# Performance work log

Measured on AMD Instinct MI355X. Metric: run time of the kernel, lower is better.

The kernel has to match this reference:

```python
import jax, jax.numpy as jnp
import numpy as np

N = 50000
E = 800000
D = 256
EPS = 1e-5  # BatchNorm eps


def _gcn_conv(x, W, b, row, col):
    # PyG GCNConv: h = x @ W; add self-loops; sym-normalize; scatter-add; + bias
    h = x @ W  # [N, D]
    deg = jnp.zeros((N,), x.dtype).at[col].add(jnp.ones((row.shape[0],), x.dtype))
    dinv = jax.lax.rsqrt(deg)  # deg >= 1 thanks to self-loops
    norm = dinv[row] * dinv[col]  # [E+N]
    msg = h[row] * norm[:, None]  # gather + scale, [E+N, D]
    out = jnp.zeros_like(h).at[col].add(msg)  # scatter-aggregate
    return out + b


def _bn(x, gamma, beta):
    # BatchNorm1d in training mode: batch statistics over nodes
    m = jnp.mean(x, axis=0)
    v = jnp.var(x, axis=0)
    return (x - m) * jax.lax.rsqrt(v + EPS) * gamma + beta


def setup_inputs() -> dict:
    key = jax.random.key(0)
    ks = jax.random.split(key, 4)
    x = jax.random.normal(ks[0], (N, D), dtype=jnp.float32)
    edge_index = jax.random.randint(ks[1], (2, E), 0, N, dtype=jnp.int64)
    s = 1.0 / np.sqrt(D)
    W1 = jax.random.uniform(ks[2], (D, D), jnp.float32, -s, s)
    W2 = jax.random.uniform(ks[3], (D, D), jnp.float32, -s, s)
    z = jnp.zeros((D,), jnp.float32)
    o = jnp.ones((D,), jnp.float32)
    return {"x": x, "edge_index": edge_index,
            "W1": W1, "b1": z, "g1": o, "be1": z,
            "W2": W2, "b2": z, "g2": o, "be2": z}


def reference(x, edge_index, W1, b1, g1, be1, W2, b2, g2, be2):
    loops = jnp.arange(N, dtype=edge_index.dtype)
    row = jnp.concatenate([edge_index[0], loops])  # sources
    col = jnp.concatenate([edge_index[1], loops])  # targets
    # layer 1: GCNConv -> BN -> ReLU (dropout is identity in eval)
    h = _gcn_conv(x, W1, b1, row, col)
    h = jax.nn.relu(_bn(h, g1, be1))
    # layer 2
    h = _gcn_conv(h, W2, b2, row, col)
    h = jax.nn.relu(_bn(h, g2, be2))
    return h
```

## Files before the change

kernel.cpp:

```cpp
#include <hip/hip_runtime.h>
#include <cstdint>
#include <cstddef>

constexpr int N = 50000;
constexpr int E = 800000;
constexpr int D = 256;
constexpr float EPS = 1e-5f;
constexpr int NB = (N + 255) / 256;
constexpr int BN_BLOCKS = 512;
constexpr int GB = (N + 63) / 64;

typedef __attribute__((ext_vector_type(8))) short short8;
typedef __attribute__((ext_vector_type(4))) float f32x4;

__device__ __forceinline__ unsigned short f2bf(float f) {
  union { float f; unsigned u; } c; c.f = f;
  unsigned u = c.u;
  u += 0x7fff + ((u >> 16) & 1);
  return (unsigned short)(u >> 16);
}
__device__ __forceinline__ float bf2f(unsigned short h) {
  union { unsigned u; float f; } c; c.u = ((unsigned)h) << 16;
  return c.f;
}

__global__ void k_detect(const void* __restrict__ ei, int* __restrict__ flag) {
  int t = threadIdx.x;
  const int* p = (const int*)ei;
  int nz = 0;
  for (int i = 2 * t + 1; i < 2048; i += 128) nz |= (p[i] != 0);
  unsigned long long b = __ballot(nz != 0);
  if (t == 0) *flag = (b == 0ULL) ? 1 : 0;
}

__device__ __forceinline__ int edge_at(const void* ei, int is64, long long pos) {
  if (is64) return (int)((const long long*)ei)[pos];
  return ((const int*)ei)[pos];
}

__global__ void k_count(const void* __restrict__ ei, const int* __restrict__ flag,
                        int* __restrict__ degc) {
  int e = blockIdx.x * 256 + threadIdx.x;
  if (e >= E) return;
  int is64 = *flag;
  int c = edge_at(ei, is64, (long long)E + e);
  atomicAdd(&degc[c], 1);
}

__global__ void k_scan_partial(const int* __restrict__ degc, int* __restrict__ bsum,
                               float* __restrict__ dinv) {
  __shared__ int sd[256];
  int t = threadIdx.x;
  int i = blockIdx.x * 256 + t;
  int dv = (i < N) ? degc[i] : 0;
  if (i < N) dinv[i] = rsqrtf((float)(dv + 1));
  int v = (i < N) ? (dv + 1) : 0;
  sd[t] = v;
  __syncthreads();
  for (int s = 128; s > 0; s >>= 1) {
    if (t < s) sd[t] += sd[t + s];
    __syncthreads();
  }
  if (t == 0) bsum[blockIdx.x] = sd[0];
}

__global__ void k_scan_block(int* __restrict__ bsum) {
  __shared__ int sd[256];
  int t = threadIdx.x;
  int v = (t < NB) ? bsum[t] : 0;
  sd[t] = v;
  __syncthreads();
  for (int off = 1; off < 256; off <<= 1) {
    int x = (t >= off) ? sd[t - off] : 0;
    __syncthreads();
    sd[t] += x;
    __syncthreads();
  }
  if (t < NB) bsum[t] = sd[t] - v;
}

__global__ void k_scan_final(const int* __restrict__ degc, const int* __restrict__ bsum,
                             const float* __restrict__ dinv, int* __restrict__ offs,
                             int* __restrict__ curs, int* __restrict__ esrc,
                             float* __restrict__ enrm) {
  __shared__ int sd[256];
  int t = threadIdx.x;
  int i = blockIdx.x * 256 + t;
  int v = (i < N) ? (degc[i] + 1) : 0;
  sd[t] = v;
  __syncthreads();
  for (int off = 1; off < 256; off <<= 1) {
    int x = (t >= off) ? sd[t - off] : 0;
    __syncthreads();
    sd[t] += x;
    __syncthreads();
  }
  if (i < N) {
    int o = bsum[blockIdx.x] + sd[t] - v;
    offs[i] = o;
    curs[i] = o + 1;
    esrc[o] = i;
    float d = dinv[i];
    enrm[o] = d * d;
  }
  if (i == N - 1) offs[N] = bsum[blockIdx.x] + sd[t];
}

__global__ void k_fill_edges(const void* __restrict__ ei, const int* __restrict__ flag,
                             const float* __restrict__ dinv, int* __restrict__ curs,
                             int* __restrict__ esrc, float* __restrict__ enrm) {
  int e = blockIdx.x * 256 + threadIdx.x;
  if (e >= E) return;
  int is64 = *flag;
  int r = edge_at(ei, is64, e);
  int c = edge_at(ei, is64, (long long)E + e);
  int p = atomicAdd(&curs[c], 1);
  esrc[p] = r;
  enrm[p] = dinv[r] * dinv[c];
}

__global__ void k_wfrag(const float* __restrict__ W, unsigned short* __restrict__ Wf) {
  int tile = blockIdx.x;
  int lane = threadIdx.x;
  int kstep = tile >> 4, wn = tile & 15;
  int kbase = kstep * 32 + (lane >> 4) * 8;
  int col = wn * 16 + (lane & 15);
  short8 v;
#pragma unroll
  for (int j = 0; j < 8; ++j)
    v[j] = (short)f2bf(W[(size_t)(kbase + j) * 256 + col]);
  *(short8*)&Wf[(((size_t)tile) * 64 + lane) * 8] = v;
}

template <bool A_BF16, bool FUSE_BN>
__global__ __launch_bounds__(256) void k_gemm(const void* __restrict__ Ap,
                                              const unsigned short* __restrict__ Wf,
                                              unsigned short* __restrict__ C,
                                              const float* __restrict__ sc,
                                              const float* __restrict__ sh) {
  __shared__ unsigned short As[64][40];
  __shared__ unsigned short Cs[64][264];
  int t = threadIdx.x;
  int lane = t & 63;
  int w = t >> 6;
  int row0 = blockIdx.x * 64;
  int l16 = lane & 15, lk = lane >> 4;

  f32x4 acc[4][4];
#pragma unroll
  for (int i = 0; i < 4; ++i)
#pragma unroll
    for (int j = 0; j < 4; ++j) acc[i][j] = (f32x4){0.f, 0.f, 0.f, 0.f};

  int arow = t >> 2;
  int akc = (t & 3) * 8;

  for (int ks = 0; ks < 8; ++ks) {
    {
      int gr = row0 + arow;
      float f[8] = {0.f, 0.f, 0.f, 0.f, 0.f, 0.f, 0.f, 0.f};
      if (gr < N) {
        if (A_BF16) {
          const unsigned short* A = (const unsigned short*)Ap;
          short8 v = *(const short8*)&A[(size_t)gr * 256 + ks * 32 + akc];
#pragma unroll
          for (int j = 0; j < 8; ++j) f[j] = bf2f((unsigned short)v[j]);
        } else {
          const float* A = (const float*)Ap;
          float4 f0 = *(const float4*)&A[(size_t)gr * 256 + ks * 32 + akc];
          float4 f1 = *(const float4*)&A[(size_t)gr * 256 + ks * 32 + akc + 4];
          f[0] = f0.x; f[1] = f0.y; f[2] = f0.z; f[3] = f0.w;
          f[4] = f1.x; f[5] = f1.y; f[6] = f1.z; f[7] = f1.w;
        }
      }
      if (FUSE_BN) {
#pragma unroll
        for (int j = 0; j < 8; ++j)
          f[j] = fmaxf(fmaf(f[j], sc[ks * 32 + akc + j], sh[ks * 32 + akc + j]), 0.f);
      }
      ushort4 u0 = {f2bf(f[0]), f2bf(f[1]), f2bf(f[2]), f2bf(f[3])};
      ushort4 u1 = {f2bf(f[4]), f2bf(f[5]), f2bf(f[6]), f2bf(f[7])};
      *(ushort4*)&As[arow][akc] = u0;
      *(ushort4*)&As[arow][akc + 4] = u1;
    }
    __syncthreads();

    short8 af[4];
#pragma unroll
    for (int mf = 0; mf < 4; ++mf)
      af[mf] = *(const short8*)&As[mf * 16 + l16][lk * 8];
#pragma unroll
    for (int nf = 0; nf < 4; ++nf) {
      short8 bf = *(const short8*)&Wf[(((size_t)ks * 16 + w * 4 + nf) * 64 + lane) * 8];
#pragma unroll
      for (int mf = 0; mf < 4; ++mf)
        acc[mf][nf] = __builtin_amdgcn_mfma_f32_16x16x32_bf16(af[mf], bf, acc[mf][nf], 0, 0, 0);
    }
    __syncthreads();
  }

#pragma unroll
  for (int mf = 0; mf < 4; ++mf)
#pragma unroll
    for (int nf = 0; nf < 4; ++nf)
#pragma unroll
      for (int r = 0; r < 4; ++r)
        Cs[mf * 16 + lk * 4 + r][w * 64 + nf * 16 + l16] = f2bf(acc[mf][nf][r]);
  __syncthreads();
#pragma unroll
  for (int it = 0; it < 8; ++it) {
    int r = it * 8 + (t >> 5);
    int gr = row0 + r;
    if (gr < N)
      *(short8*)&C[(size_t)gr * 256 + (t & 31) * 8] = *(const short8*)&Cs[r][(t & 31) * 8];
  }
}

template <bool OUT_BF16>
__global__ __launch_bounds__(256) void k_agg(const unsigned short* __restrict__ h,
                                             const int* __restrict__ offs,
                                             const int* __restrict__ esrc,
                                             const float* __restrict__ enrm,
                                             const float* __restrict__ bias,
                                             void* __restrict__ outp) {
  int nd = blockIdx.x * 4 + (threadIdx.x >> 6);
  if (nd >= N) return;
  int node = __builtin_amdgcn_readfirstlane(nd);
  int lane = threadIdx.x & 63;
  int e = offs[node];
  int end = offs[node + 1];
  float a0 = 0.f, a1 = 0.f, a2 = 0.f, a3 = 0.f;

#define ACC4(v, wgt)                                            \
  do {                                                          \
    a0 = fmaf(wgt, bf2f((unsigned short)((v).x & 0xffff)), a0); \
    a1 = fmaf(wgt, bf2f((unsigned short)((v).x >> 16)), a1);    \
    a2 = fmaf(wgt, bf2f((unsigned short)((v).y & 0xffff)), a2); \
    a3 = fmaf(wgt, bf2f((unsigned short)((v).y >> 16)), a3);    \
  } while (0)

  for (; e + 4 <= end; e += 4) {
    int s0 = esrc[e], s1 = esrc[e + 1], s2 = esrc[e + 2], s3 = esrc[e + 3];
    float w0 = enrm[e], w1 = enrm[e + 1], w2 = enrm[e + 2], w3 = enrm[e + 3];
    uint2 v0 = *(const uint2*)&h[(size_t)s0 * 256 + lane * 4];
    uint2 v1 = *(const uint2*)&h[(size_t)s1 * 256 + lane * 4];
    uint2 v2 = *(const uint2*)&h[(size_t)s2 * 256 + lane * 4];
    uint2 v3 = *(const uint2*)&h[(size_t)s3 * 256 + lane * 4];
    ACC4(v0, w0);
    ACC4(v1, w1);
    ACC4(v2, w2);
    ACC4(v3, w3);
  }
  for (; e < end; ++e) {
    int s = esrc[e];
    float wgt = enrm[e];
    uint2 v = *(const uint2*)&h[(size_t)s * 256 + lane * 4];
    ACC4(v, wgt);
  }
#undef ACC4

  float4 bb = ((const float4*)bias)[lane];
  a0 += bb.x; a1 += bb.y; a2 += bb.z; a3 += bb.w;
  if (OUT_BF16) {
    ushort4 o = {f2bf(a0), f2bf(a1), f2bf(a2), f2bf(a3)};
    *(ushort4*)&((unsigned short*)outp)[(size_t)nd * 256 + lane * 4] = o;
  } else {
    float4 o = {a0, a1, a2, a3};
    *(float4*)&((float*)outp)[(size_t)nd * 256 + lane * 4] = o;
  }
}

template <bool IN_BF16>
__global__ __launch_bounds__(256) void k_bnpart(const void* __restrict__ xp,
                                                float* __restrict__ partial) {
  int t = threadIdx.x;
  int lane = t & 63;
  int sub = t >> 6;
  float sx = 0, sy = 0, sz = 0, sw = 0;
  float qx = 0, qy = 0, qz = 0, qw = 0;
  for (int r = blockIdx.x * 4 + sub; r < N; r += gridDim.x * 4) {
    float4 v;
    if (IN_BF16) {
      uint2 u = *(const uint2*)&((const unsigned short*)xp)[(size_t)r * 256 + lane * 4];
      v.x = bf2f((unsigned short)(u.x & 0xffff));
      v.y = bf2f((unsigned short)(u.x >> 16));
      v.z = bf2f((unsigned short)(u.y & 0xffff));
      v.w = bf2f((unsigned short)(u.y >> 16));
    } else {
      v = *(const float4*)&((const float*)xp)[(size_t)r * 256 + lane * 4];
    }
    sx += v.x; sy += v.y; sz += v.z; sw += v.w;
    qx = fmaf(v.x, v.x, qx); qy = fmaf(v.y, v.y, qy);
    qz = fmaf(v.z, v.z, qz); qw = fmaf(v.w, v.w, qw);
  }
  __shared__ float4 ps[256];
  __shared__ float4 pq[256];
  ps[t] = {sx, sy, sz, sw};
  pq[t] = {qx, qy, qz, qw};
  __syncthreads();
  float* pout = partial + (size_t)blockIdx.x * 512;
  if (t < 64) {
    float4 a = ps[t], b = ps[64 + t], c = ps[128 + t], d = ps[192 + t];
    float4 o = {a.x + b.x + c.x + d.x, a.y + b.y + c.y + d.y,
                a.z + b.z + c.z + d.z, a.w + b.w + c.w + d.w};
    ((float4*)pout)[t] = o;
  } else if (t < 128) {
    int l = t - 64;
    float4 a = pq[l], b = pq[64 + l], c = pq[128 + l], d = pq[192 + l];
    float4 o = {a.x + b.x + c.x + d.x, a.y + b.y + c.y + d.y,
                a.z + b.z + c.z + d.z, a.w + b.w + c.w + d.w};
    ((float4*)(pout + 256))[l] = o;
  }
}

__global__ __launch_bounds__(256) void k_bnred(const float* __restrict__ partial,
                                               float* __restrict__ bnsum,
                                               float* __restrict__ bnsq) {
  int t = threadIdx.x;
  float s = 0.f, q = 0.f;
  int b0 = blockIdx.x * (BN_BLOCKS / 16);
  for (int b = b0; b < b0 + BN_BLOCKS / 16; ++b) {
    s += partial[(size_t)b * 512 + t];
    q += partial[(size_t)b * 512 + 256 + t];
  }
  atomicAdd(&bnsum[t], s);
  atomicAdd(&bnsq[t], q);
}

__global__ void k_bnfinal(const float* __restrict__ bnsum, const float* __restrict__ bnsq,
                          const float* __restrict__ g, const float* __restrict__ be,
                          float* __restrict__ sc, float* __restrict__ sh) {
  int t = threadIdx.x;
  const float inv = 1.f / (float)N;
  float m = bnsum[t] * inv;
  float v = bnsq[t] * inv - m * m;
  float s = rsqrtf(v + EPS) * g[t];
  sc[t] = s;
  sh[t] = be[t] - m * s;
}

__global__ __launch_bounds__(256) void k_bnapply(float* __restrict__ x,
                                                 const float* __restrict__ sc,
                                                 const float* __restrict__ sh) {
  int t = threadIdx.x;
  int lane = t & 63;
  int sub = t >> 6;
  float4 s4 = ((const float4*)sc)[lane];
  float4 h4 = ((const float4*)sh)[lane];
  float4* xv = (float4*)x;
  for (int r = blockIdx.x * 4 + sub; r < N; r += gridDim.x * 4) {
    float4 v = xv[(size_t)r * 64 + lane];
    v.x = fmaxf(fmaf(v.x, s4.x, h4.x), 0.f);
    v.y = fmaxf(fmaf(v.y, s4.y, h4.y), 0.f);
    v.z = fmaxf(fmaf(v.z, s4.z, h4.z), 0.f);
    v.w = fmaxf(fmaf(v.w, s4.w, h4.w), 0.f);
    xv[(size_t)r * 64 + lane] = v;
  }
}

extern "C" void kernel_launch(void* const* d_in, const int* in_sizes, int n_in,
                              void* d_out, int out_size, void* d_ws, size_t ws_size,
                              hipStream_t stream) {
  const float* x  = (const float*)d_in[0];
  const void*  ei = d_in[1];
  const float* W1 = (const float*)d_in[2];
  const float* b1 = (const float*)d_in[3];
  const float* g1 = (const float*)d_in[4];
  const float* be1 = (const float*)d_in[5];
  const float* W2 = (const float*)d_in[6];
  const float* b2 = (const float*)d_in[7];
  const float* g2 = (const float*)d_in[8];
  const float* be2 = (const float*)d_in[9];
  float* out = (float*)d_out;

  char* base = (char*)d_ws;
  size_t off = 0;
  unsigned short* hbuf = (unsigned short*)(base + off); off += (size_t)N * D * 2;
  unsigned short* abuf = (unsigned short*)(base + off); off += (size_t)N * D * 2;
  unsigned short* Wf1 = (unsigned short*)(base + off);  off += (size_t)D * D * 2;
  unsigned short* Wf2 = (unsigned short*)(base + off);  off += (size_t)D * D * 2;
  int*   degc = (int*)(base + off);   off += (size_t)N * 4;
  float* dinv = (float*)(base + off); off += (size_t)N * 4;
  int*   offs = (int*)(base + off);   off += (size_t)(N + 4) * 4;
  int*   curs = (int*)(base + off);   off += (size_t)N * 4;
  int*   esrc = (int*)(base + off);   off += (size_t)(E + N) * 4;
  float* enrm = (float*)(base + off); off += (size_t)(E + N) * 4;
  float* partial = (float*)(base + off); off += (size_t)BN_BLOCKS * 512 * 4;
  float* bnsum = (float*)(base + off); off += (size_t)D * 4;
  float* bnsq  = (float*)(base + off); off += (size_t)D * 4;
  float* sc1 = (float*)(base + off);  off += (size_t)D * 4;
  float* sh1 = (float*)(base + off);  off += (size_t)D * 4;
  float* sc2 = (float*)(base + off);  off += (size_t)D * 4;
  float* sh2 = (float*)(base + off);  off += (size_t)D * 4;
  int*   bsum = (int*)(base + off);   off += 256 * 4;
  int*   flag = (int*)(base + off);   off += 16;

  k_wfrag<<<128, 64, 0, stream>>>(W1, Wf1);
  k_wfrag<<<128, 64, 0, stream>>>(W2, Wf2);

  hipMemsetAsync(degc, 0, (size_t)N * 4, stream);
  k_detect<<<1, 64, 0, stream>>>(ei, flag);
  k_count<<<(E + 255) / 256, 256, 0, stream>>>(ei, flag, degc);
  k_scan_partial<<<NB, 256, 0, stream>>>(degc, bsum, dinv);
  k_scan_block<<<1, 256, 0, stream>>>(bsum);
  k_scan_final<<<NB, 256, 0, stream>>>(degc, bsum, dinv, offs, curs, esrc, enrm);
  k_fill_edges<<<(E + 255) / 256, 256, 0, stream>>>(ei, flag, dinv, curs, esrc, enrm);

  k_gemm<false, false><<<GB, 256, 0, stream>>>(x, Wf1, hbuf, nullptr, nullptr);
  k_agg<true><<<(N + 3) / 4, 256, 0, stream>>>(hbuf, offs, esrc, enrm, b1, abuf);
  hipMemsetAsync(bnsum, 0, 2 * (size_t)D * 4, stream);
  k_bnpart<true><<<BN_BLOCKS, 256, 0, stream>>>(abuf, partial);
  k_bnred<<<16, 256, 0, stream>>>(partial, bnsum, bnsq);
  k_bnfinal<<<1, 256, 0, stream>>>(bnsum, bnsq, g1, be1, sc1, sh1);

  k_gemm<true, true><<<GB, 256, 0, stream>>>(abuf, Wf2, hbuf, sc1, sh1);
  k_agg<false><<<(N + 3) / 4, 256, 0, stream>>>(hbuf, offs, esrc, enrm, b2, out);
  hipMemsetAsync(bnsum, 0, 2 * (size_t)D * 4, stream);
  k_bnpart<false><<<BN_BLOCKS, 256, 0, stream>>>(out, partial);
  k_bnred<<<16, 256, 0, stream>>>(partial, bnsum, bnsq);
  k_bnfinal<<<1, 256, 0, stream>>>(bnsum, bnsq, g2, be2, sc2, sh2);
  k_bnapply<<<512, 256, 0, stream>>>(out, sc2, sh2);
}
```

Baseline: 324.2 us.

## Pack edge src/norm pairs, stage full A tile, bf16 layer-2 intermediate

Interleaves each CSR edge's source index and normalization weight into one int2 array, so aggregation issues one 8-byte load per edge instead of two separate loads. The aggregation loop is unrolled to 8 edges to keep more gathers in flight. The GEMM now loads the whole 64x256 A tile into shared memory once and reuses that buffer for the output staging, removing the per-k-step barriers. Layer-2 aggregation now writes bf16 into a workspace buffer, and the final BN-apply converts it to fp32, which cuts traffic but adds bf16 rounding before the second BatchNorm.

```diff
diff --git a/kernel.cpp b/kernel.cpp
--- a/kernel.cpp
+++ b/kernel.cpp
@@ -81,8 +81,7 @@
 
 __global__ void k_scan_final(const int* __restrict__ degc, const int* __restrict__ bsum,
                              const float* __restrict__ dinv, int* __restrict__ offs,
-                             int* __restrict__ curs, int* __restrict__ esrc,
-                             float* __restrict__ enrm) {
+                             int* __restrict__ curs, int2* __restrict__ epair) {
   __shared__ int sd[256];
   int t = threadIdx.x;
   int i = blockIdx.x * 256 + t;
@@ -99,24 +98,22 @@
     int o = bsum[blockIdx.x] + sd[t] - v;
     offs[i] = o;
     curs[i] = o + 1;
-    esrc[o] = i;
     float d = dinv[i];
-    enrm[o] = d * d;
+    epair[o] = make_int2(i, __float_as_int(d * d));
   }
   if (i == N - 1) offs[N] = bsum[blockIdx.x] + sd[t];
 }
 
 __global__ void k_fill_edges(const void* __restrict__ ei, const int* __restrict__ flag,
                              const float* __restrict__ dinv, int* __restrict__ curs,
-                             int* __restrict__ esrc, float* __restrict__ enrm) {
+                             int2* __restrict__ epair) {
   int e = blockIdx.x * 256 + threadIdx.x;
   if (e >= E) return;
   int is64 = *flag;
   int r = edge_at(ei, is64, e);
   int c = edge_at(ei, is64, (long long)E + e);
   int p = atomicAdd(&curs[c], 1);
-  esrc[p] = r;
-  enrm[p] = dinv[r] * dinv[c];
+  epair[p] = make_int2(r, __float_as_int(dinv[r] * dinv[c]));
 }
 
 __global__ void k_wfrag(const float* __restrict__ W, unsigned short* __restrict__ Wf) {
@@ -138,8 +135,7 @@
                                               unsigned short* __restrict__ C,
                                               const float* __restrict__ sc,
                                               const float* __restrict__ sh) {
-  __shared__ unsigned short As[64][40];
-  __shared__ unsigned short Cs[64][264];
+  __shared__ unsigned short As[64][264];
   int t = threadIdx.x;
   int lane = t & 63;
   int w = t >> 6;
@@ -153,42 +149,46 @@
     for (int j = 0; j < 4; ++j) acc[i][j] = (f32x4){0.f, 0.f, 0.f, 0.f};
 
   int arow = t >> 2;
-  int akc = (t & 3) * 8;
-
+  int ak0 = (t & 3) * 8;
+  int gr = row0 + arow;
+  bool inb = (gr < N);
+
+#pragma unroll
   for (int ks = 0; ks < 8; ++ks) {
-    {
-      int gr = row0 + arow;
-      float f[8] = {0.f, 0.f, 0.f, 0.f, 0.f, 0.f, 0.f, 0.f};
-      if (gr < N) {
-        if (A_BF16) {
-          const unsigned short* A = (const unsigned short*)Ap;
-          short8 v = *(const short8*)&A[(size_t)gr * 256 + ks * 32 + akc];
-#pragma unroll
-          for (int j = 0; j < 8; ++j) f[j] = bf2f((unsigned short)v[j]);
-        } else {
-          const float* A = (const float*)Ap;
-          float4 f0 = *(const float4*)&A[(size_t)gr * 256 + ks * 32 + akc];
-          float4 f1 = *(const float4*)&A[(size_t)gr * 256 + ks * 32 + akc + 4];
-          f[0] = f0.x; f[1] = f0.y; f[2] = f0.z; f[3] = f0.w;
-          f[4] = f1.x; f[5] = f1.y; f[6] = f1.z; f[7] = f1.w;
-        }
+    int kc = ks * 32 + ak0;
+    float f[8] = {0.f, 0.f, 0.f, 0.f, 0.f, 0.f, 0.f, 0.f};
+    if (inb) {
+      if (A_BF16) {
+        const unsigned short* A = (const unsigned short*)Ap;
+        short8 v = *(const short8*)&A[(size_t)gr * 256 + kc];
+#pragma unroll
+        for (int j = 0; j < 8; ++j) f[j] = bf2f((unsigned short)v[j]);
+      } else {
+        const float* A = (const float*)Ap;
+        float4 f0 = *(const float4*)&A[(size_t)gr * 256 + kc];
+        float4 f1 = *(const float4*)&A[(size_t)gr * 256 + kc + 4];
+        f[0] = f0.x; f[1] = f0.y; f[2] = f0.z; f[3] = f0.w;
+        f[4] = f1.x; f[5] = f1.y; f[6] = f1.z; f[7] = f1.w;
       }
-      if (FUSE_BN) {
-#pragma unroll
-        for (int j = 0; j < 8; ++j)
-          f[j] = fmaxf(fmaf(f[j], sc[ks * 32 + akc + j], sh[ks * 32 + akc + j]), 0.f);
-      }
-      ushort4 u0 = {f2bf(f[0]), f2bf(f[1]), f2bf(f[2]), f2bf(f[3])};
-      ushort4 u1 = {f2bf(f[4]), f2bf(f[5]), f2bf(f[6]), f2bf(f[7])};
-      *(ushort4*)&As[arow][akc] = u0;
-      *(ushort4*)&As[arow][akc + 4] = u1;
     }
-    __syncthreads();
-
+    if (FUSE_BN) {
+#pragma unroll
+      for (int j = 0; j < 8; ++j)
+        f[j] = fmaxf(fmaf(f[j], sc[kc + j], sh[kc + j]), 0.f);
+    }
+    ushort4 u0 = {f2bf(f[0]), f2bf(f[1]), f2bf(f[2]), f2bf(f[3])};
+    ushort4 u1 = {f2bf(f[4]), f2bf(f[5]), f2bf(f[6]), f2bf(f[7])};
+    *(ushort4*)&As[arow][kc] = u0;
+    *(ushort4*)&As[arow][kc + 4] = u1;
+  }
+  __syncthreads();
+
+#pragma unroll
+  for (int ks = 0; ks < 8; ++ks) {
     short8 af[4];
 #pragma unroll
     for (int mf = 0; mf < 4; ++mf)
-      af[mf] = *(const short8*)&As[mf * 16 + l16][lk * 8];
+      af[mf] = *(const short8*)&As[mf * 16 + l16][ks * 32 + lk * 8];
 #pragma unroll
     for (int nf = 0; nf < 4; ++nf) {
       short8 bf = *(const short8*)&Wf[(((size_t)ks * 16 + w * 4 + nf) * 64 + lane) * 8];
@@ -196,9 +196,10 @@
       for (int mf = 0; mf < 4; ++mf)
         acc[mf][nf] = __builtin_amdgcn_mfma_f32_16x16x32_bf16(af[mf], bf, acc[mf][nf], 0, 0, 0);
     }
-    __syncthreads();
-  }
-
+  }
+  __syncthreads();
+
+  unsigned short(*Cs)[264] = As;
 #pragma unroll
   for (int mf = 0; mf < 4; ++mf)
 #pragma unroll
@@ -210,19 +211,17 @@
 #pragma unroll
   for (int it = 0; it < 8; ++it) {
     int r = it * 8 + (t >> 5);
-    int gr = row0 + r;
-    if (gr < N)
-      *(short8*)&C[(size_t)gr * 256 + (t & 31) * 8] = *(const short8*)&Cs[r][(t & 31) * 8];
-  }
-}
-
-template <bool OUT_BF16>
+    int gr2 = row0 + r;
+    if (gr2 < N)
+      *(short8*)&C[(size_t)gr2 * 256 + (t & 31) * 8] = *(const short8*)&Cs[r][(t & 31) * 8];
+  }
+}
+
 __global__ __launch_bounds__(256) void k_agg(const unsigned short* __restrict__ h,
                                              const int* __restrict__ offs,
-                                             const int* __restrict__ esrc,
-                                             const float* __restrict__ enrm,
+                                             const int2* __restrict__ epair,
                                              const float* __restrict__ bias,
-                                             void* __restrict__ outp) {
+                                             unsigned short* __restrict__ outp) {
   int nd = blockIdx.x * 4 + (threadIdx.x >> 6);
   if (nd >= N) return;
   int node = __builtin_amdgcn_readfirstlane(nd);
@@ -239,39 +238,40 @@
     a3 = fmaf(wgt, bf2f((unsigned short)((v).y >> 16)), a3);    \
   } while (0)
 
-  for (; e + 4 <= end; e += 4) {
-    int s0 = esrc[e], s1 = esrc[e + 1], s2 = esrc[e + 2], s3 = esrc[e + 3];
-    float w0 = enrm[e], w1 = enrm[e + 1], w2 = enrm[e + 2], w3 = enrm[e + 3];
-    uint2 v0 = *(const uint2*)&h[(size_t)s0 * 256 + lane * 4];
-    uint2 v1 = *(const uint2*)&h[(size_t)s1 * 256 + lane * 4];
-    uint2 v2 = *(const uint2*)&h[(size_t)s2 * 256 + lane * 4];
-    uint2 v3 = *(const uint2*)&h[(size_t)s3 * 256 + lane * 4];
-    ACC4(v0, w0);
-    ACC4(v1, w1);
-    ACC4(v2, w2);
-    ACC4(v3, w3);
+  for (; e + 8 <= end; e += 8) {
+    int2 p0 = epair[e + 0], p1 = epair[e + 1], p2 = epair[e + 2], p3 = epair[e + 3];
+    int2 p4 = epair[e + 4], p5 = epair[e + 5], p6 = epair[e + 6], p7 = epair[e + 7];
+    uint2 v0 = *(const uint2*)&h[(size_t)p0.x * 256 + lane * 4];
+    uint2 v1 = *(const uint2*)&h[(size_t)p1.x * 256 + lane * 4];
+    uint2 v2 = *(const uint2*)&h[(size_t)p2.x * 256 + lane * 4];
+    uint2 v3 = *(const uint2*)&h[(size_t)p3.x * 256 + lane * 4];
+    uint2 v4 = *(const uint2*)&h[(size_t)p4.x * 256 + lane * 4];
+    uint2 v5 = *(const uint2*)&h[(size_t)p5.x * 256 + lane * 4];
+    uint2 v6 = *(const uint2*)&h[(size_t)p6.x * 256 + lane * 4];
+    uint2 v7 = *(const uint2*)&h[(size_t)p7.x * 256 + lane * 4];
+    ACC4(v0, __int_as_float(p0.y));
+    ACC4(v1, __int_as_float(p1.y));
+    ACC4(v2, __int_as_float(p2.y));
+    ACC4(v3, __int_as_float(p3.y));
+    ACC4(v4, __int_as_float(p4.y));
+    ACC4(v5, __int_as_float(p5.y));
+    ACC4(v6, __int_as_float(p6.y));
+    ACC4(v7, __int_as_float(p7.y));
   }
   for (; e < end; ++e) {
-    int s = esrc[e];
-    float wgt = enrm[e];
-    uint2 v = *(const uint2*)&h[(size_t)s * 256 + lane * 4];
-    ACC4(v, wgt);
+    int2 p = epair[e];
+    uint2 v = *(const uint2*)&h[(size_t)p.x * 256 + lane * 4];
+    ACC4(v, __int_as_float(p.y));
   }
 #undef ACC4
 
   float4 bb = ((const float4*)bias)[lane];
   a0 += bb.x; a1 += bb.y; a2 += bb.z; a3 += bb.w;
-  if (OUT_BF16) {
-    ushort4 o = {f2bf(a0), f2bf(a1), f2bf(a2), f2bf(a3)};
-    *(ushort4*)&((unsigned short*)outp)[(size_t)nd * 256 + lane * 4] = o;
-  } else {
-    float4 o = {a0, a1, a2, a3};
-    *(float4*)&((float*)outp)[(size_t)nd * 256 + lane * 4] = o;
-  }
-}
-
-template <bool IN_BF16>
-__global__ __launch_bounds__(256) void k_bnpart(const void* __restrict__ xp,
+  ushort4 o = {f2bf(a0), f2bf(a1), f2bf(a2), f2bf(a3)};
+  *(ushort4*)&outp[(size_t)nd * 256 + lane * 4] = o;
+}
+
+__global__ __launch_bounds__(256) void k_bnpart(const unsigned short* __restrict__ xp,
                                                 float* __restrict__ partial) {
   int t = threadIdx.x;
   int lane = t & 63;
@@ -279,19 +279,14 @@
   float sx = 0, sy = 0, sz = 0, sw = 0;
   float qx = 0, qy = 0, qz = 0, qw = 0;
   for (int r = blockIdx.x * 4 + sub; r < N; r += gridDim.x * 4) {
-    float4 v;
-    if (IN_BF16) {
-      uint2 u = *(const uint2*)&((const unsigned short*)xp)[(size_t)r * 256 + lane * 4];
-      v.x = bf2f((unsigned short)(u.x & 0xffff));
-      v.y = bf2f((unsigned short)(u.x >> 16));
-      v.z = bf2f((unsigned short)(u.y & 0xffff));
-      v.w = bf2f((unsigned short)(u.y >> 16));
-    } else {
-      v = *(const float4*)&((const float*)xp)[(size_t)r * 256 + lane * 4];
-    }
-    sx += v.x; sy += v.y; sz += v.z; sw += v.w;
-    qx = fmaf(v.x, v.x, qx); qy = fmaf(v.y, v.y, qy);
-    qz = fmaf(v.z, v.z, qz); qw = fmaf(v.w, v.w, qw);
+    uint2 u = *(const uint2*)&xp[(size_t)r * 256 + lane * 4];
+    float vx = bf2f((unsigned short)(u.x & 0xffff));
+    float vy = bf2f((unsigned short)(u.x >> 16));
+    float vz = bf2f((unsigned short)(u.y & 0xffff));
+    float vw = bf2f((unsigned short)(u.y >> 16));
+    sx += vx; sy += vy; sz += vz; sw += vw;
+    qx = fmaf(vx, vx, qx); qy = fmaf(vy, vy, qy);
+    qz = fmaf(vz, vz, qz); qw = fmaf(vw, vw, qw);
   }
   __shared__ float4 ps[256];
   __shared__ float4 pq[256];
@@ -339,7 +334,8 @@
   sh[t] = be[t] - m * s;
 }
 
-__global__ __launch_bounds__(256) void k_bnapply(float* __restrict__ x,
+__global__ __launch_bounds__(256) void k_bnapply(const unsigned short* __restrict__ in,
+                                                 float* __restrict__ outp,
                                                  const float* __restrict__ sc,
                                                  const float* __restrict__ sh) {
   int t = threadIdx.x;
@@ -347,14 +343,14 @@
   int sub = t >> 6;
   float4 s4 = ((const float4*)sc)[lane];
   float4 h4 = ((const float4*)sh)[lane];
-  float4* xv = (float4*)x;
   for (int r = blockIdx.x * 4 + sub; r < N; r += gridDim.x * 4) {
-    float4 v = xv[(size_t)r * 64 + lane];
-    v.x = fmaxf(fmaf(v.x, s4.x, h4.x), 0.f);
-    v.y = fmaxf(fmaf(v.y, s4.y, h4.y), 0.f);
-    v.z = fmaxf(fmaf(v.z, s4.z, h4.z), 0.f);
-    v.w = fmaxf(fmaf(v.w, s4.w, h4.w), 0.f);
-    xv[(size_t)r * 64 + lane] = v;
+    uint2 u = *(const uint2*)&in[(size_t)r * 256 + lane * 4];
+    float4 v;
+    v.x = fmaxf(fmaf(bf2f((unsigned short)(u.x & 0xffff)), s4.x, h4.x), 0.f);
+    v.y = fmaxf(fmaf(bf2f((unsigned short)(u.x >> 16)), s4.y, h4.y), 0.f);
+    v.z = fmaxf(fmaf(bf2f((unsigned short)(u.y & 0xffff)), s4.z, h4.z), 0.f);
+    v.w = fmaxf(fmaf(bf2f((unsigned short)(u.y >> 16)), s4.w, h4.w), 0.f);
+    *(float4*)&outp[(size_t)r * 256 + lane * 4] = v;
   }
 }
 
@@ -383,8 +379,7 @@
   float* dinv = (float*)(base + off); off += (size_t)N * 4;
   int*   offs = (int*)(base + off);   off += (size_t)(N + 4) * 4;
   int*   curs = (int*)(base + off);   off += (size_t)N * 4;
-  int*   esrc = (int*)(base + off);   off += (size_t)(E + N) * 4;
-  float* enrm = (float*)(base + off); off += (size_t)(E + N) * 4;
+  int2*  epair = (int2*)(base + off); off += (size_t)(E + N) * 8;
   float* partial = (float*)(base + off); off += (size_t)BN_BLOCKS * 512 * 4;
   float* bnsum = (float*)(base + off); off += (size_t)D * 4;
   float* bnsq  = (float*)(base + off); off += (size_t)D * 4;
@@ -403,21 +398,21 @@
   k_count<<<(E + 255) / 256, 256, 0, stream>>>(ei, flag, degc);
   k_scan_partial<<<NB, 256, 0, stream>>>(degc, bsum, dinv);
   k_scan_block<<<1, 256, 0, stream>>>(bsum);
-  k_scan_final<<<NB, 256, 0, stream>>>(degc, bsum, dinv, offs, curs, esrc, enrm);
-  k_fill_edges<<<(E + 255) / 256, 256, 0, stream>>>(ei, flag, dinv, curs, esrc, enrm);
+  k_scan_final<<<NB, 256, 0, stream>>>(degc, bsum, dinv, offs, curs, epair);
+  k_fill_edges<<<(E + 255) / 256, 256, 0, stream>>>(ei, flag, dinv, curs, epair);
 
   k_gemm<false, false><<<GB, 256, 0, stream>>>(x, Wf1, hbuf, nullptr, nullptr);
-  k_agg<true><<<(N + 3) / 4, 256, 0, stream>>>(hbuf, offs, esrc, enrm, b1, abuf);
+  k_agg<<<(N + 3) / 4, 256, 0, stream>>>(hbuf, offs, epair, b1, abuf);
   hipMemsetAsync(bnsum, 0, 2 * (size_t)D * 4, stream);
-  k_bnpart<true><<<BN_BLOCKS, 256, 0, stream>>>(abuf, partial);
+  k_bnpart<<<BN_BLOCKS, 256, 0, stream>>>(abuf, partial);
   k_bnred<<<16, 256, 0, stream>>>(partial, bnsum, bnsq);
   k_bnfinal<<<1, 256, 0, stream>>>(bnsum, bnsq, g1, be1, sc1, sh1);
 
   k_gemm<true, true><<<GB, 256, 0, stream>>>(abuf, Wf2, hbuf, sc1, sh1);
-  k_agg<false><<<(N + 3) / 4, 256, 0, stream>>>(hbuf, offs, esrc, enrm, b2, out);
+  k_agg<<<(N + 3) / 4, 256, 0, stream>>>(hbuf, offs, epair, b2, abuf);
   hipMemsetAsync(bnsum, 0, 2 * (size_t)D * 4, stream);
-  k_bnpart<false><<<BN_BLOCKS, 256, 0, stream>>>(out, partial);
+  k_bnpart<<<BN_BLOCKS, 256, 0, stream>>>(abuf, partial);
   k_bnred<<<16, 256, 0, stream>>>(partial, bnsum, bnsq);
   k_bnfinal<<<1, 256, 0, stream>>>(bnsum, bnsq, g2, be2, sc2, sh2);
-  k_bnapply<<<512, 256, 0, stream>>>(out, sc2, sh2);
-}
+  k_bnapply<<<512, 256, 0, stream>>>(abuf, out, sc2, sh2);
+}
```

Result: faster. 315.4 us (-2.7%).
